# Optimization experiments

Hardware: AMD Instinct MI355X
Metric: run time of the kernel (lower is better)

The kernel has to match this reference:

```python
import jax, jax.numpy as jnp
import numpy as np

S, B, F, D, DF, NH, FH = 1152, 2, 128, 1024, 2048, 8, 4
SEP = 1024
EPS = 1e-5

def ln(x, g, b):
    m = x.mean(-1, keepdims=True)
    v = ((x - m) ** 2).mean(-1, keepdims=True)
    return (x - m) * jax.lax.rsqrt(v + EPS) * g + b

def mha(q, k, v, wi, bi, wo, bo, nh):
    # torch MultiheadAttention, batch_first=False: inputs (L, N, E)
    E = q.shape[-1]
    hd = E // nh
    qh = (q @ wi[:E].T + bi[:E]).reshape(q.shape[0], -1, nh, hd)
    kh = (k @ wi[E:2 * E].T + bi[E:2 * E]).reshape(k.shape[0], -1, nh, hd)
    vh = (v @ wi[2 * E:].T + bi[2 * E:]).reshape(k.shape[0], -1, nh, hd)
    s = jnp.einsum('qnhd,knhd->nhqk', qh, kh) / jnp.sqrt(jnp.float32(hd))
    a = jax.nn.softmax(s, axis=-1)
    o = jnp.einsum('nhqk,knhd->qnhd', a, vh).reshape(q.shape[0], -1, E)
    return o @ wo.T + bo

def setup_inputs() -> dict:
    key = jax.random.key(0)
    it = iter(jax.random.split(key, 40))
    def p(shape, s=0.02):
        return jax.random.normal(next(it), shape, jnp.float32) * s
    z = lambda *sh: jnp.zeros(sh, jnp.float32)
    o = lambda *sh: jnp.ones(sh, jnp.float32)
    return dict(
        src=jax.random.normal(next(it), (S, B, F), jnp.float32),
        sep=SEP,
        sa_wi=p((3 * D, D)), sa_bi=z(3 * D), sa_wo=p((D, D)), sa_bo=z(D),
        fa_wi=p((3 * F, F)), fa_bi=z(3 * F), fa_wo=p((F, F)), fa_bo=z(F),
        pl1_w=p((F, 1)), pl1_b=z(F),
        pl2_w=p((DF, F)), pl2_b=z(DF),
        pl3_w=p((1, DF)), pl3_b=z(1),
        pl4_w=p((DF, F)), pl4_b=z(DF),
        pl5_w=p((D, DF)), pl5_b=z(D),
        pl6_w=p((DF, D)), pl6_b=z(DF),
        pl7_w=p((D, DF)), pl7_b=z(D),
        l1_w=p((DF, D)), l1_b=z(DF),
        l2_w=p((F, DF)), l2_b=z(F),
        pn1_g=o(F), pn1_b=z(F),
        pn2_g=o(D), pn2_b=z(D),
        n1_g=o(D), n1_b=z(D),
        n2_g=o(F), n2_b=z(F),
    )

def _forward(src, sa_wi, sa_bi, sa_wo, sa_bo, fa_wi, fa_bi, fa_wo, fa_bo,
             pl1_w, pl1_b, pl2_w, pl2_b, pl3_w, pl3_b, pl4_w, pl4_b,
             pl5_w, pl5_b, pl6_w, pl6_b, pl7_w, pl7_b, l1_w, l1_b, l2_w, l2_b,
             pn1_g, pn1_b, pn2_g, pn2_b, n1_g, n1_b, n2_g, n2_b, sep):
    Sn, Bn, Fn = src.shape
    relu = jax.nn.relu
    # feature-wise attention: 'b h w -> w (b h) 1'
    x = jnp.transpose(src, (2, 0, 1)).reshape(Fn, Sn * Bn, 1)
    x = x @ pl1_w.T + pl1_b                       # (F, S*B, emsize_f)
    x = mha(x, x, x, fa_wi, fa_bi, fa_wo, fa_bo, FH)
    x = relu(x @ pl2_w.T + pl2_b) @ pl3_w.T + pl3_b  # (F, S*B, 1)
    x = jnp.transpose(x.reshape(Fn, Sn, Bn), (1, 2, 0))  # 'w (b h) 1 -> b h w'
    src1 = ln(x + src, pn1_g, pn1_b)              # (S, B, F)
    src1_ = relu(src1 @ pl4_w.T + pl4_b) @ pl5_w.T + pl5_b  # (S, B, D)
    li = src1_[:sep]
    sl = mha(li, li, li, sa_wi, sa_bi, sa_wo, sa_bo, NH)
    sl = ln(sl + li, pn2_g, pn2_b)
    sl_ = relu(sl @ pl6_w.T + pl6_b) @ pl7_w.T + pl7_b
    sl_ = ln(sl_, pn2_g, pn2_b) + sl
    sr = mha(src1_[sep:], sl_, sl_, sa_wi, sa_bi, sa_wo, sa_bo, NH)
    src2 = jnp.concatenate([sl, sr], axis=0)      # (S, B, D)
    so = ln(src2 + src1_, n1_g, n1_b)
    ff = relu(so @ l1_w.T + l1_b) @ l2_w.T + l2_b  # (S, B, F)
    return ln(src1 + ff, n2_g, n2_b)

def reference(src, sa_wi, sa_bi, sa_wo, sa_bo, fa_wi, fa_bi, fa_wo, fa_bo,
              pl1_w, pl1_b, pl2_w, pl2_b, pl3_w, pl3_b, pl4_w, pl4_b,
              pl5_w, pl5_b, pl6_w, pl6_b, pl7_w, pl7_b, l1_w, l1_b, l2_w, l2_b,
              pn1_g, pn1_b, pn2_g, pn2_b, n1_g, n1_b, n2_g, n2_b, sep):
    return _forward(src, sa_wi, sa_bi, sa_wo, sa_bo, fa_wi, fa_bi, fa_wo, fa_bo,
                    pl1_w, pl1_b, pl2_w, pl2_b, pl3_w, pl3_b, pl4_w, pl4_b,
                    pl5_w, pl5_b, pl6_w, pl6_b, pl7_w, pl7_b, l1_w, l1_b,
                    l2_w, l2_b, pn1_g, pn1_b, pn2_g, pn2_b, n1_g, n1_b,
                    n2_g, n2_b, sep)
```

## Files before the change

### kernel.cpp

```cpp
#include <hip/hip_runtime.h>

using s16x8 = __attribute__((ext_vector_type(8))) short;
using f32x4 = __attribute__((ext_vector_type(4))) float;
typedef unsigned short ushort_t;

__device__ __forceinline__ unsigned short f2bf(float f) {
    union { float f; unsigned u; } v; v.f = f;
    unsigned u = v.u + 0x7FFFu + ((v.u >> 16) & 1u);
    return (unsigned short)(u >> 16);
}
__device__ __forceinline__ float bf2f(unsigned short h) {
    union { unsigned u; float f; } v; v.u = ((unsigned)h) << 16;
    return v.f;
}

__device__ __forceinline__ float block_reduce(float v, int op, float* lds) {
    const int lane = threadIdx.x & 63;
    const int w    = threadIdx.x >> 6;
    const int nw   = blockDim.x >> 6;
#pragma unroll
    for (int off = 32; off > 0; off >>= 1) {
        float o = __shfl_down(v, off, 64);
        v = op ? fmaxf(v, o) : (v + o);
    }
    __syncthreads();
    if (lane == 0) lds[w] = v;
    __syncthreads();
    float r = lds[0];
    for (int i = 1; i < nw; i++) r = op ? fmaxf(r, lds[i]) : (r + lds[i]);
    return r;
}

__device__ __forceinline__ void load_lds16(const void* g, void* l) {
    __builtin_amdgcn_global_load_lds(
        (const __attribute__((address_space(1))) unsigned int*)g,
        (__attribute__((address_space(3))) unsigned int*)l, 16, 0, 0);
}

struct CvtArgs { const float* src[8]; ushort_t* dst[8]; int end[8]; };

__global__ __launch_bounds__(256)
void cvt_all(CvtArgs a)
{
    int i = blockIdx.x * 256 + threadIdx.x;
    int j = 0;
    while (j < 8 && i >= a.end[j]) j++;
    if (j >= 8) return;
    int li = i - (j ? a.end[j - 1] : 0);
    float4 v = *(const float4*)&a.src[j][(size_t)li * 4];
    ushort_t u[4] = { f2bf(v.x), f2bf(v.y), f2bf(v.z), f2bf(v.w) };
    *(uint2*)&a.dst[j][(size_t)li * 4] = *(uint2*)u;
}

template<bool RELU, bool SPLITK>
__global__ __launch_bounds__(256, 2)
void gemm_bf16(const ushort_t* __restrict__ A, const ushort_t* __restrict__ B,
               const float* __restrict__ bias, ushort_t* __restrict__ C,
               float* __restrict__ Cp, long pstride, int ksplen, int zmod,
               int M, int N, int K, int lda, int ldb, int ldc,
               long sAz, long sBz, long sCz, long sA2, long sB2, long sC2,
               int zshift, float alpha)
{
    __shared__ ushort_t As[128 * 32];
    __shared__ ushort_t Bs[128 * 32];

    const int tid = threadIdx.x;
    int zz = blockIdx.z;
    int ks = 0, z = zz;
    if (SPLITK) { ks = zz / zmod; z = zz - ks * zmod; }
    const int z1  = z & ((1 << zshift) - 1);
    const int z2  = z >> zshift;
    const int m0  = blockIdx.x * 128;
    const int n0  = blockIdx.y * 128;

    const ushort_t* Ab = A + (size_t)z1 * sAz + (size_t)z2 * sA2 + (size_t)m0 * lda;
    const ushort_t* Bb = B + (size_t)z1 * sBz + (size_t)z2 * sB2 + (size_t)n0 * ldb;

    const int wave = tid >> 6, lane = tid & 63;
    const int wm = (wave & 1) * 64, wn = (wave >> 1) * 64;
    const int mi = lane & 15, quad = lane >> 4;

    f32x4 acc[4][4];
#pragma unroll
    for (int i = 0; i < 4; i++)
#pragma unroll
        for (int j = 0; j < 4; j++) acc[i][j] = (f32x4)0.f;

    const int r_0 = tid >> 2,           g_0 = (tid & 3) ^ ((r_0 >> 1) & 3);
    const int r_1 = (tid + 256) >> 2,   g_1 = (tid & 3) ^ ((r_1 >> 1) & 3);

    const int kbeg = SPLITK ? ks * ksplen : 0;
    const int kend = SPLITK ? kbeg + ksplen : K;

    for (int k0 = kbeg; k0 < kend; k0 += 32) {
        load_lds16(Ab + (size_t)r_0 * lda + k0 + g_0 * 8, &As[tid * 8]);
        load_lds16(Ab + (size_t)r_1 * lda + k0 + g_1 * 8, &As[(tid + 256) * 8]);
        load_lds16(Bb + (size_t)r_0 * ldb + k0 + g_0 * 8, &Bs[tid * 8]);
        load_lds16(Bb + (size_t)r_1 * ldb + k0 + g_1 * 8, &Bs[(tid + 256) * 8]);
        __syncthreads();

        s16x8 af[4], bfr[4];
#pragma unroll
        for (int t = 0; t < 4; t++) {
            int r = wm + t * 16 + mi;
            af[t] = *(const s16x8*)&As[r * 32 + ((quad ^ ((r >> 1) & 3)) * 8)];
        }
#pragma unroll
        for (int t = 0; t < 4; t++) {
            int r = wn + t * 16 + mi;
            bfr[t] = *(const s16x8*)&Bs[r * 32 + ((quad ^ ((r >> 1) & 3)) * 8)];
        }
#pragma unroll
        for (int tm = 0; tm < 4; tm++)
#pragma unroll
            for (int tn = 0; tn < 4; tn++)
                acc[tm][tn] = __builtin_amdgcn_mfma_f32_16x16x32_bf16(af[tm], bfr[tn], acc[tm][tn], 0, 0, 0);
        __syncthreads();
    }

    if (SPLITK) {
        float* Cf = Cp + (size_t)ks * pstride + (size_t)z1 * sCz + (size_t)z2 * sC2;
#pragma unroll
        for (int tn = 0; tn < 4; tn++) {
            int col = n0 + wn + tn * 16 + mi;
#pragma unroll
            for (int tm = 0; tm < 4; tm++)
#pragma unroll
                for (int r = 0; r < 4; r++) {
                    int row = m0 + wm + tm * 16 + quad * 4 + r;
                    Cf[(size_t)row * ldc + col] = acc[tm][tn][r] * alpha;
                }
        }
    } else {
#pragma unroll
        for (int tn = 0; tn < 4; tn++) {
            int col = n0 + wn + tn * 16 + mi;
            float bv = bias ? bias[col] : 0.f;
#pragma unroll
            for (int tm = 0; tm < 4; tm++) {
#pragma unroll
                for (int r = 0; r < 4; r++) {
                    int row = m0 + wm + tm * 16 + quad * 4 + r;
                    float v = acc[tm][tn][r] * alpha + bv;
                    if (RELU) v = fmaxf(v, 0.f);
                    C[(size_t)z1 * sCz + (size_t)z2 * sC2 + (size_t)row * ldc + col] = f2bf(v);
                }
            }
        }
    }
}

__global__ __launch_bounds__(256)
void sum_cvt(const float* __restrict__ parts, long pstride, int P,
             const float* __restrict__ bias, int ldc,
             ushort_t* __restrict__ out, int total4)
{
    int i = blockIdx.x * 256 + threadIdx.x;
    if (i >= total4) return;
    size_t idx = (size_t)i * 4;
    float4 s = *(const float4*)&parts[idx];
    for (int p = 1; p < P; p++) {
        float4 v = *(const float4*)&parts[(size_t)p * pstride + idx];
        s.x += v.x; s.y += v.y; s.z += v.z; s.w += v.w;
    }
    if (bias) {
        int col = (int)(idx % (size_t)ldc);
        s.x += bias[col]; s.y += bias[col + 1]; s.z += bias[col + 2]; s.w += bias[col + 3];
    }
    ushort_t u[4] = { f2bf(s.x), f2bf(s.y), f2bf(s.z), f2bf(s.w) };
    *(uint2*)&out[idx] = *(uint2*)u;
}

__global__ __launch_bounds__(128)
void ln_part(const float* __restrict__ parts, long pstride, int P,
             const float* __restrict__ bias, const ushort_t* __restrict__ resid,
             const float* __restrict__ g, const float* __restrict__ beta,
             float* __restrict__ out)
{
    __shared__ float red[4];
    const int r = blockIdx.x, c = threadIdx.x;
    float x = bias[c] + bf2f(resid[r * 128 + c]);
    for (int p = 0; p < P; p++) x += parts[(size_t)p * pstride + (size_t)r * 128 + c];
    float s  = block_reduce(x, 0, red);
    float ss = block_reduce(x * x, 0, red);
    float mean = s * (1.f / 128.f);
    float var  = ss * (1.f / 128.f) - mean * mean;
    float inv  = rsqrtf(var + 1e-5f);
    out[(size_t)r * 128 + c] = (x - mean) * inv * g[c] + beta[c];
}

__global__ __launch_bounds__(256)
void transp128(const ushort_t* __restrict__ in, ushort_t* __restrict__ out,
               int ldin, long inz1, long inz2, long outz)
{
    __shared__ ushort_t T[64][136];
    const int z = blockIdx.z, z1 = z & 7, z2 = z >> 3;
    const int n0 = blockIdx.x * 64;
    const ushort_t* ip = in + (size_t)z1 * inz1 + (size_t)z2 * inz2;
    const int rr = threadIdx.x >> 2, cg = (threadIdx.x & 3) * 32;
#pragma unroll
    for (int c = 0; c < 4; c++) {
        s16x8 v = *(const s16x8*)(ip + (size_t)(n0 + rr) * ldin + cg + c * 8);
        *(s16x8*)&T[rr][cg + c * 8] = v;
    }
    __syncthreads();
    const int d = threadIdx.x >> 1, j0 = (threadIdx.x & 1) * 32;
    ushort_t* op = out + (size_t)z * outz + (size_t)d * 1024 + n0 + j0;
#pragma unroll
    for (int c = 0; c < 4; c++) {
        s16x8 v;
#pragma unroll
        for (int j = 0; j < 8; j++) v[j] = (short)T[j0 + c * 8 + j][d];
        *(s16x8*)(op + c * 8) = v;
    }
}

__global__ void precomp1(const float* __restrict__ fa_wi, const float* __restrict__ fa_bi,
                         const float* __restrict__ pl1_w, const float* __restrict__ pl1_b,
                         float* __restrict__ consts)
{
    int j = threadIdx.x;
    if (j < 384) {
        float u = 0.f, v = 0.f;
        for (int k = 0; k < 128; k++) {
            float w = fa_wi[j * 128 + k];
            u = fmaf(w, pl1_w[k], u);
            v = fmaf(w, pl1_b[k], v);
        }
        consts[j]       = u;
        consts[512 + j] = v + fa_bi[j];
    }
}

__global__ void precomp2(const float* __restrict__ fa_wo, const float* __restrict__ fa_bo,
                         float* __restrict__ consts)
{
    int tid = threadIdx.x;
    const float* u = consts;
    const float* v = consts + 512;
    if (tid < 16) {
        int h = tid >> 2, w = tid & 3;
        const float* ql = (w < 2) ? u : v;
        const float* kr = ((w & 1) == 0) ? u : v;
        float acc = 0.f;
        for (int d = 0; d < 32; d++) acc += ql[h * 32 + d] * kr[128 + h * 32 + d];
        consts[1024 + tid] = acc * 0.17677669529663687f;
    }
#pragma unroll
    for (int h = 0; h < 4; h++) {
        float acc = 0.f;
        for (int d = 0; d < 32; d++)
            acc = fmaf(fa_wo[tid * 128 + h * 32 + d], u[256 + h * 32 + d], acc);
        consts[1088 + h * 128 + tid] = acc;
    }
    float c0 = fa_bo[tid];
    for (int idx = 0; idx < 128; idx++)
        c0 = fmaf(fa_wo[tid * 128 + idx], v[256 + idx], c0);
    consts[1600 + tid] = c0;
}

__global__ void precomp3(const float* __restrict__ pl2_w, const float* __restrict__ pl2_b,
                         const float* __restrict__ consts, ushort_t* __restrict__ Gb)
{
    int m = blockIdx.x * 256 + threadIdx.x;
    const float* wv = consts + 1088;
    const float* c0 = consts + 1600;
    float a0 = 0.f, ah[4] = {0.f, 0.f, 0.f, 0.f};
    for (int j = 0; j < 128; j++) {
        float w = pl2_w[m * 128 + j];
        ah[0] = fmaf(w, wv[0 * 128 + j], ah[0]);
        ah[1] = fmaf(w, wv[1 * 128 + j], ah[1]);
        ah[2] = fmaf(w, wv[2 * 128 + j], ah[2]);
        ah[3] = fmaf(w, wv[3 * 128 + j], ah[3]);
        a0    = fmaf(w, c0[j], a0);
    }
    ushort_t row[8];
#pragma unroll
    for (int h = 0; h < 4; h++) row[h] = f2bf(ah[h]);
    row[4] = f2bf(a0 + pl2_b[m]);
    row[5] = row[6] = row[7] = 0;
    *(uint4*)&Gb[m * 8] = *(uint4*)row;
}

__global__ __launch_bounds__(512, 4)
void feat_mlp_ln(const float* __restrict__ src, const float* __restrict__ consts,
                 const ushort_t* __restrict__ Gb, const float* __restrict__ pl3_w,
                 const float* __restrict__ pl3_b, const float* __restrict__ pn1_g,
                 const float* __restrict__ pn1_b, ushort_t* __restrict__ src1)
{
    __shared__ ushort_t Gs[2048 * 8];
    __shared__ ushort_t Ts[128 * 8];
    __shared__ float    sv[128];
    __shared__ float    ypart[4][128];
    __shared__ float    red[8];

    const int n   = blockIdx.x;
    const int tid = threadIdx.x;
    const int f   = tid & 127;
    const int h   = tid >> 7;
    const bool act = (tid < 128);

#pragma unroll
    for (int p = 0; p < 4; p++) {
        int ci = tid + p * 512;
        load_lds16(Gb + (size_t)ci * 8, &Gs[ci * 8]);
    }
    if (act) sv[f] = src[n * 128 + f];
    __syncthreads();

    const float si = sv[f];
    float S1 = block_reduce(act ? si : 0.f, 0, red);
    float S2 = block_reduce(act ? si * si : 0.f, 0, red);
    float S3 = block_reduce(act ? si * si * si : 0.f, 0, red);
    float S4 = block_reduce(act ? si * si * si * si : 0.f, 0, red);
    float amax = block_reduce(act ? fabsf(si) : 0.f, 1, red);

    const float p_ = consts[1024 + h * 4 + 0] * si + consts[1024 + h * 4 + 2];
    float pmax = block_reduce(fabsf(p_), 1, red);

    float tt;
    if (pmax * amax < 0.25f) {
        float num = fmaf(p_, fmaf(p_, fmaf(p_, S4 * (1.f / 6.f), 0.5f * S3), S2), S1);
        float den = fmaf(p_, fmaf(p_, fmaf(p_, S3 * (1.f / 6.f), 0.5f * S2), S1), 128.f);
        tt = num / den;
    } else {
        float smax = block_reduce(act ? si : -3.4e38f, 1, red);
        float smin = -block_reduce(act ? -si : -3.4e38f, 1, red);
        float m = fmaxf(p_ * smax, p_ * smin);
        float l = 0.f, t = 0.f;
        for (int j = 0; j < 128; j++) {
            float e = __expf(fmaf(p_, sv[j], -m));
            l += e; t = fmaf(e, sv[j], t);
        }
        tt = t / l;
    }

    Ts[f * 8 + h] = f2bf(tt);
    if (act) {
        Ts[f * 8 + 4] = 0x3F80;
        Ts[f * 8 + 5] = 0; Ts[f * 8 + 6] = 0; Ts[f * 8 + 7] = 0;
    }
    __syncthreads();

    const int wave = tid >> 6, lane = tid & 63;
    const int wm = (wave & 1) * 64;
    const int mq = wave >> 1;
    const int mi = lane & 15, quad = lane >> 4;

    s16x8 af[4];
#pragma unroll
    for (int t = 0; t < 4; t++) {
        s16x8 v = *(const s16x8*)&Ts[(wm + t * 16 + mi) * 8];
        af[t] = (quad == 0) ? v : (s16x8)0;
    }

    float partial[4][4];
#pragma unroll
    for (int i = 0; i < 4; i++)
#pragma unroll
        for (int j = 0; j < 4; j++) partial[i][j] = 0.f;

#pragma unroll 4
    for (int mt = 0; mt < 32; mt++) {
        const int m0 = mq * 512 + mt * 16;
        s16x8 bfr = *(const s16x8*)&Gs[(m0 + mi) * 8];
        float w = pl3_w[m0 + mi];
        f32x4 acc[4];
#pragma unroll
        for (int tm = 0; tm < 4; tm++)
            acc[tm] = __builtin_amdgcn_mfma_f32_16x16x32_bf16(af[tm], bfr, (f32x4)0.f, 0, 0, 0);
#pragma unroll
        for (int tm = 0; tm < 4; tm++)
#pragma unroll
            for (int r = 0; r < 4; r++)
                partial[tm][r] = fmaf(fmaxf(acc[tm][r], 0.f), w, partial[tm][r]);
    }

#pragma unroll
    for (int tm = 0; tm < 4; tm++)
#pragma unroll
        for (int r = 0; r < 4; r++) {
            float v = partial[tm][r];
            v += __shfl_xor(v, 8);
            v += __shfl_xor(v, 4);
            v += __shfl_xor(v, 2);
            v += __shfl_xor(v, 1);
            if (mi == 0) ypart[mq][wm + tm * 16 + quad * 4 + r] = v;
        }
    __syncthreads();

    float yv = 0.f;
    if (act)
        yv = ypart[0][f] + ypart[1][f] + ypart[2][f] + ypart[3][f] + pl3_b[0] + sv[f];
    float s  = block_reduce(yv, 0, red);
    float ss = block_reduce(yv * yv, 0, red);
    float mean = s * (1.f / 128.f);
    float var  = ss * (1.f / 128.f) - mean * mean;
    float inv  = rsqrtf(var + 1e-5f);
    if (act)
        src1[n * 128 + f] = f2bf((yv - mean) * inv * pn1_g[f] + pn1_b[f]);
}

template<bool OUTF32>
__global__ void ln_bf16(const ushort_t* __restrict__ a, const ushort_t* __restrict__ b,
                        const ushort_t* __restrict__ post, const float* __restrict__ g,
                        const float* __restrict__ beta, void* __restrict__ out, int D)
{
    __shared__ float red[4];
    const size_t row = blockIdx.x;
    const int tid = threadIdx.x;
    const int nit = D / blockDim.x;
    const ushort_t* ap = a + row * D;
    const ushort_t* bp = b ? b + row * D : nullptr;
    float xr[4];
    float s = 0.f, ss = 0.f;
    for (int i = 0; i < nit; i++) {
        int idx = i * blockDim.x + tid;
        float x = bf2f(ap[idx]) + (bp ? bf2f(bp[idx]) : 0.f);
        xr[i] = x; s += x; ss = fmaf(x, x, ss);
    }
    s  = block_reduce(s, 0, red);
    ss = block_reduce(ss, 0, red);
    float mean = s / D, var = ss / D - mean * mean;
    float inv = rsqrtf(var + 1e-5f);
    const ushort_t* pp = post ? post + row * D : nullptr;
    for (int i = 0; i < nit; i++) {
        int idx = i * blockDim.x + tid;
        float v = (xr[i] - mean) * inv * g[idx] + beta[idx];
        if (pp) v += bf2f(pp[idx]);
        if (OUTF32) ((float*)out)[row * D + idx] = v;
        else        ((ushort_t*)out)[row * D + idx] = f2bf(v);
    }
}

__global__ void ln_cat(const ushort_t* __restrict__ a1, const ushort_t* __restrict__ a2,
                       int split, const ushort_t* __restrict__ b,
                       const float* __restrict__ g, const float* __restrict__ beta,
                       ushort_t* __restrict__ out, int D)
{
    __shared__ float red[4];
    const int row = blockIdx.x;
    const int tid = threadIdx.x;
    const int nit = D / blockDim.x;
    const ushort_t* ap = (row < split) ? a1 + (size_t)row * D : a2 + (size_t)(row - split) * D;
    const ushort_t* bp = b + (size_t)row * D;
    float xr[4];
    float s = 0.f, ss = 0.f;
    for (int i = 0; i < nit; i++) {
        int idx = i * blockDim.x + tid;
        float x = bf2f(ap[idx]) + bf2f(bp[idx]);
        xr[i] = x; s += x; ss = fmaf(x, x, ss);
    }
    s  = block_reduce(s, 0, red);
    ss = block_reduce(ss, 0, red);
    float mean = s / D, var = ss / D - mean * mean;
    float inv = rsqrtf(var + 1e-5f);
    for (int i = 0; i < nit; i++) {
        int idx = i * blockDim.x + tid;
        out[(size_t)row * D + idx] = f2bf((xr[i] - mean) * inv * g[idx] + beta[idx]);
    }
}

__global__ __launch_bounds__(256)
void softmax_bf16(ushort_t* __restrict__ S)
{
    __shared__ float red[4];
    const size_t row = blockIdx.x;
    ushort_t* p = S + row * 1024;
    const int tid = threadIdx.x;
    uint2 u = *(const uint2*)&p[tid * 4];
    ushort_t* us = (ushort_t*)&u;
    float xr[4];
    float mx = -3.4e38f;
#pragma unroll
    for (int i = 0; i < 4; i++) { xr[i] = bf2f(us[i]); mx = fmaxf(mx, xr[i]); }
    mx = block_reduce(mx, 1, red);
    float sum = 0.f;
#pragma unroll
    for (int i = 0; i < 4; i++) { xr[i] = __expf(xr[i] - mx); sum += xr[i]; }
    sum = block_reduce(sum, 0, red);
    float inv = 1.f / sum;
#pragma unroll
    for (int i = 0; i < 4; i++) us[i] = f2bf(xr[i] * inv);
    *(uint2*)&p[tid * 4] = u;
}

static inline void gemm_go(hipStream_t s, const ushort_t* A, const ushort_t* B,
                           const float* bias, ushort_t* C,
                           int M, int N, int K, int lda, int ldb, int ldc,
                           long sAz, long sBz, long sCz, int Z, float alpha,
                           bool relu,
                           long sA2 = 0, long sB2 = 0, long sC2 = 0, int zshift = 0,
                           int ksplit = 1, float* Cp = nullptr, long pstride = 0)
{
    dim3 g(M / 128, N / 128, Z * ksplit), b(256);
    int ksplen = K / ksplit;
    if (ksplit > 1)
        gemm_bf16<false, true ><<<g, b, 0, s>>>(A, B, nullptr, nullptr, Cp, pstride, ksplen, Z,
            M, N, K, lda, ldb, ldc, sAz, sBz, sCz, sA2, sB2, sC2, zshift, alpha);
    else if (relu)
        gemm_bf16<true,  false><<<g, b, 0, s>>>(A, B, bias, C, nullptr, 0, 0, Z,
            M, N, K, lda, ldb, ldc, sAz, sBz, sCz, sA2, sB2, sC2, zshift, alpha);
    else
        gemm_bf16<false, false><<<g, b, 0, s>>>(A, B, bias, C, nullptr, 0, 0, Z,
            M, N, K, lda, ldb, ldc, sAz, sBz, sCz, sA2, sB2, sC2, zshift, alpha);
}

extern "C" void kernel_launch(void* const* d_in, const int* in_sizes, int n_in,
                              void* d_out, int out_size, void* d_ws, size_t ws_size,
                              hipStream_t stream)
{
    const float* src   = (const float*)d_in[0];
    const float* sa_wi = (const float*)d_in[2];
    const float* sa_bi = (const float*)d_in[3];
    const float* sa_wo = (const float*)d_in[4];
    const float* sa_bo = (const float*)d_in[5];
    const float* fa_wi = (const float*)d_in[6];
    const float* fa_bi = (const float*)d_in[7];
    const float* fa_wo = (const float*)d_in[8];
    const float* fa_bo = (const float*)d_in[9];
    const float* pl1_w = (const float*)d_in[10];
    const float* pl1_b = (const float*)d_in[11];
    const float* pl2_w = (const float*)d_in[12];
    const float* pl2_b = (const float*)d_in[13];
    const float* pl3_w = (const float*)d_in[14];
    const float* pl3_b = (const float*)d_in[15];
    const float* pl4_w = (const float*)d_in[16];
    const float* pl4_b = (const float*)d_in[17];
    const float* pl5_w = (const float*)d_in[18];
    const float* pl5_b = (const float*)d_in[19];
    const float* pl6_w = (const float*)d_in[20];
    const float* pl6_b = (const float*)d_in[21];
    const float* pl7_w = (const float*)d_in[22];
    const float* pl7_b = (const float*)d_in[23];
    const float* l1_w  = (const float*)d_in[24];
    const float* l1_b  = (const float*)d_in[25];
    const float* l2_w  = (const float*)d_in[26];
    const float* l2_b  = (const float*)d_in[27];
    const float* pn1_g = (const float*)d_in[28];
    const float* pn1_b = (const float*)d_in[29];
    const float* pn2_g = (const float*)d_in[30];
    const float* pn2_b = (const float*)d_in[31];
    const float* n1_g  = (const float*)d_in[32];
    const float* n1_b  = (const float*)d_in[33];
    const float* n2_g  = (const float*)d_in[34];
    const float* n2_b  = (const float*)d_in[35];

    float* ws  = (float*)d_ws;
    float* out = (float*)d_out;

    float* CONSTS = ws;
    ushort_t* wsb = (ushort_t*)(ws + 16384);
    ushort_t* SAWIb  = wsb + 0;
    ushort_t* SAWOb  = wsb + 3145728;
    ushort_t* PL4b   = wsb + 4194304;
    ushort_t* PL5b   = wsb + 4456448;
    ushort_t* PL6b   = wsb + 6553600;
    ushort_t* PL7b   = wsb + 8650752;
    ushort_t* L1b    = wsb + 10747904;
    ushort_t* L2b    = wsb + 12845056;
    ushort_t* Gbb    = wsb + 13107200;
    ushort_t* SRC1b  = wsb + 13172736;
    ushort_t* HBIGb  = wsb + 13467648;
    ushort_t* SRC1_b = wsb + 18186240;
    ushort_t* QKVb   = wsb + 20545536;
    ushort_t* SBUFb  = wsb + 27623424;
    ushort_t* OBUFb  = wsb + 44400640;
    ushort_t* SLb    = wsb + 46497792;
    ushort_t* SLPb   = wsb + 48594944;
    ushort_t* SOb    = wsb + 50692096;
    float* PARTS = (float*)SBUFb;

    {
        CvtArgs a;
        const float* srcs[8] = { sa_wi, sa_wo, pl4_w, pl5_w, pl6_w, pl7_w, l1_w, l2_w };
        ushort_t*    dsts[8] = { SAWIb, SAWOb, PL4b, PL5b, PL6b, PL7b, L1b, L2b };
        int          ns[8]   = { 3145728, 1048576, 262144, 2097152, 2097152, 2097152, 2097152, 262144 };
        int cum = 0;
        for (int i = 0; i < 8; i++) { a.src[i] = srcs[i]; a.dst[i] = dsts[i]; cum += ns[i] / 4; a.end[i] = cum; }
        cvt_all<<<(cum + 255) / 256, 256, 0, stream>>>(a);
    }

    precomp1<<<1, 384, 0, stream>>>(fa_wi, fa_bi, pl1_w, pl1_b, CONSTS);
    precomp2<<<1, 128, 0, stream>>>(fa_wo, fa_bo, CONSTS);
    precomp3<<<8, 256, 0, stream>>>(pl2_w, pl2_b, CONSTS, Gbb);
    feat_mlp_ln<<<2304, 512, 0, stream>>>(src, CONSTS, Gbb, pl3_w, pl3_b, pn1_g, pn1_b, SRC1b);

    gemm_go(stream, SRC1b, PL4b, pl4_b, HBIGb, 2304, 2048, 128, 128, 128, 2048, 0, 0, 0, 1, 1.f, true);
    gemm_go(stream, HBIGb, PL5b, nullptr, nullptr, 2304, 1024, 2048, 2048, 2048, 1024, 0, 0, 0, 1, 1.f, false,
            0, 0, 0, 0, 2, PARTS, 2359296);
    sum_cvt<<<2304, 256, 0, stream>>>(PARTS, 2359296, 2, pl5_b, 1024, SRC1_b, 589824);

    gemm_go(stream, SRC1_b, SAWIb, sa_bi, QKVb, 2304, 3072, 1024, 1024, 1024, 3072, 0, 0, 0, 1, 1.f, false);
    const float iscale = 0.08838834764831845f;
    ushort_t* VT1 = HBIGb;
    transp128<<<dim3(16, 1, 16), 256, 0, stream>>>(QKVb + 2048, VT1, 6144, 128, 3072, 131072);
    gemm_go(stream, QKVb, QKVb + 1024, nullptr, SBUFb,
            1024, 1024, 128, 6144, 6144, 1024, 128, 128, 1048576, 16, iscale, false,
            3072, 3072, 8388608, 3);
    softmax_bf16<<<16384, 256, 0, stream>>>(SBUFb);
    gemm_go(stream, SBUFb, VT1, nullptr, OBUFb,
            1024, 128, 1024, 1024, 1024, 2048, 1048576, 131072, 128, 16, 1.f, false,
            8388608, 1048576, 1024, 3);
    gemm_go(stream, OBUFb, SAWOb, sa_bo, HBIGb, 2048, 1024, 1024, 1024, 1024, 1024, 0, 0, 0, 1, 1.f, false);
    ln_bf16<false><<<2048, 256, 0, stream>>>(HBIGb, SRC1_b, nullptr, pn2_g, pn2_b, SLb, 1024);

    gemm_go(stream, SLb, PL6b, pl6_b, HBIGb, 2048, 2048, 1024, 1024, 1024, 2048, 0, 0, 0, 1, 1.f, true);
    gemm_go(stream, HBIGb, PL7b, pl7_b, OBUFb, 2048, 1024, 2048, 2048, 2048, 1024, 0, 0, 0, 1, 1.f, false);
    ln_bf16<false><<<2048, 256, 0, stream>>>(OBUFb, nullptr, SLb, pn2_g, pn2_b, SLPb, 1024);

    ushort_t* KV2 = SBUFb;
    ushort_t* S2  = SBUFb + 4456448;
    ushort_t* SR  = SBUFb + 6553600;
    gemm_go(stream, SLPb, SAWIb + 1024 * 1024, sa_bi + 1024, KV2, 2048, 2048, 1024, 1024, 1024, 2048, 0, 0, 0, 1, 1.f, false);
    ushort_t* VT2 = HBIGb;
    transp128<<<dim3(16, 1, 16), 256, 0, stream>>>(KV2 + 1024, VT2, 4096, 128, 2048, 131072);
    gemm_go(stream, QKVb + 2048 * 3072, KV2, nullptr, S2,
            128, 1024, 128, 6144, 4096, 1024, 128, 128, 131072, 16, iscale, false,
            3072, 2048, 1048576, 3);
    softmax_bf16<<<2048, 256, 0, stream>>>(S2);
    gemm_go(stream, S2, VT2, nullptr, nullptr,
            128, 128, 1024, 1024, 1024, 2048, 131072, 131072, 128, 16, 1.f, false,
            1048576, 1048576, 1024, 3, 8, PARTS, 262144);
    sum_cvt<<<256, 256, 0, stream>>>(PARTS, 262144, 8, nullptr, 2048, OBUFb, 65536);
    gemm_go(stream, OBUFb, SAWOb, nullptr, nullptr, 256, 1024, 1024, 1024, 1024, 1024, 0, 0, 0, 1, 1.f, false,
            0, 0, 0, 0, 8, PARTS, 262144);
    sum_cvt<<<256, 256, 0, stream>>>(PARTS, 262144, 8, sa_bo, 1024, SR, 65536);

    ln_cat<<<2304, 256, 0, stream>>>(SLb, SR, 2048, SRC1_b, n1_g, n1_b, SOb, 1024);

    gemm_go(stream, SOb, L1b, l1_b, HBIGb, 2304, 2048, 1024, 1024, 1024, 2048, 0, 0, 0, 1, 1.f, true);
    gemm_go(stream, HBIGb, L2b, nullptr, nullptr, 2304, 128, 2048, 2048, 2048, 128, 0, 0, 0, 1, 1.f, false,
            0, 0, 0, 0, 8, PARTS, 294912);
    ln_part<<<2304, 128, 0, stream>>>(PARTS, 294912, 8, l2_b, SRC1b, n2_g, n2_b, out);
}
```

Baseline: 591.0 us.

## Split-K the mid-size GEMMs and fuse bias/ReLU into partial-sum reduction

Four more large GEMMs (attention out-projection, pl6, pl7, l1) now use split-K=2, writing fp32 partials that a templated sum_cvt kernel reduces while adding bias and an optional ReLU before converting to bf16. The aim is more workgroups per GEMM to fill the GPU. In feat_mlp_ln, pl3_w is staged into LDS, the ReLU-weighted accumulation uses packed 2-wide float ops, and the occupancy hint is raised from 4 to 6. In exchange, the split-K path adds fp32 partial writes and reads plus an extra kernel launch per GEMM, which may cost more than the added parallelism gains for GEMMs that already have many tiles.

```diff
diff --git a/kernel.cpp b/kernel.cpp
--- a/kernel.cpp
+++ b/kernel.cpp
@@ -2,6 +2,7 @@
 
 using s16x8 = __attribute__((ext_vector_type(8))) short;
 using f32x4 = __attribute__((ext_vector_type(4))) float;
+using f32x2 = __attribute__((ext_vector_type(2))) float;
 typedef unsigned short ushort_t;
 
 __device__ __forceinline__ unsigned short f2bf(float f) {
@@ -150,6 +151,7 @@
     }
 }
 
+template<bool RELU>
 __global__ __launch_bounds__(256)
 void sum_cvt(const float* __restrict__ parts, long pstride, int P,
              const float* __restrict__ bias, int ldc,
@@ -166,6 +168,10 @@
     if (bias) {
         int col = (int)(idx % (size_t)ldc);
         s.x += bias[col]; s.y += bias[col + 1]; s.z += bias[col + 2]; s.w += bias[col + 3];
+    }
+    if (RELU) {
+        s.x = fmaxf(s.x, 0.f); s.y = fmaxf(s.y, 0.f);
+        s.z = fmaxf(s.z, 0.f); s.w = fmaxf(s.w, 0.f);
     }
     ushort_t u[4] = { f2bf(s.x), f2bf(s.y), f2bf(s.z), f2bf(s.w) };
     *(uint2*)&out[idx] = *(uint2*)u;
@@ -282,13 +288,14 @@
     *(uint4*)&Gb[m * 8] = *(uint4*)row;
 }
 
-__global__ __launch_bounds__(512, 4)
+__global__ __launch_bounds__(512, 6)
 void feat_mlp_ln(const float* __restrict__ src, const float* __restrict__ consts,
                  const ushort_t* __restrict__ Gb, const float* __restrict__ pl3_w,
                  const float* __restrict__ pl3_b, const float* __restrict__ pn1_g,
                  const float* __restrict__ pn1_b, ushort_t* __restrict__ src1)
 {
     __shared__ ushort_t Gs[2048 * 8];
+    __shared__ float    wlds[2048];
     __shared__ ushort_t Ts[128 * 8];
     __shared__ float    sv[128];
     __shared__ float    ypart[4][128];
@@ -305,6 +312,7 @@
         int ci = tid + p * 512;
         load_lds16(Gb + (size_t)ci * 8, &Gs[ci * 8]);
     }
+    load_lds16(pl3_w + tid * 4, &wlds[tid * 4]);
     if (act) sv[f] = src[n * 128 + f];
     __syncthreads();
 
@@ -354,33 +362,37 @@
         af[t] = (quad == 0) ? v : (s16x8)0;
     }
 
-    float partial[4][4];
-#pragma unroll
-    for (int i = 0; i < 4; i++)
-#pragma unroll
-        for (int j = 0; j < 4; j++) partial[i][j] = 0.f;
+    f32x2 partial2[4][2];
+#pragma unroll
+    for (int i = 0; i < 4; i++) { partial2[i][0] = (f32x2)0.f; partial2[i][1] = (f32x2)0.f; }
+    const f32x2 zero2 = (f32x2)0.f;
 
 #pragma unroll 4
     for (int mt = 0; mt < 32; mt++) {
         const int m0 = mq * 512 + mt * 16;
         s16x8 bfr = *(const s16x8*)&Gs[(m0 + mi) * 8];
-        float w = pl3_w[m0 + mi];
+        float w = wlds[m0 + mi];
+        f32x2 w2 = { w, w };
         f32x4 acc[4];
 #pragma unroll
         for (int tm = 0; tm < 4; tm++)
             acc[tm] = __builtin_amdgcn_mfma_f32_16x16x32_bf16(af[tm], bfr, (f32x4)0.f, 0, 0, 0);
 #pragma unroll
-        for (int tm = 0; tm < 4; tm++)
-#pragma unroll
-            for (int r = 0; r < 4; r++)
-                partial[tm][r] = fmaf(fmaxf(acc[tm][r], 0.f), w, partial[tm][r]);
+        for (int tm = 0; tm < 4; tm++) {
+            f32x2* pa = (f32x2*)&acc[tm];
+#pragma unroll
+            for (int i = 0; i < 2; i++) {
+                f32x2 r = __builtin_elementwise_max(pa[i], zero2);
+                partial2[tm][i] = r * w2 + partial2[tm][i];
+            }
+        }
     }
 
 #pragma unroll
     for (int tm = 0; tm < 4; tm++)
 #pragma unroll
         for (int r = 0; r < 4; r++) {
-            float v = partial[tm][r];
+            float v = partial2[tm][r >> 1][r & 1];
             v += __shfl_xor(v, 8);
             v += __shfl_xor(v, 4);
             v += __shfl_xor(v, 2);
@@ -589,7 +601,7 @@
     gemm_go(stream, SRC1b, PL4b, pl4_b, HBIGb, 2304, 2048, 128, 128, 128, 2048, 0, 0, 0, 1, 1.f, true);
     gemm_go(stream, HBIGb, PL5b, nullptr, nullptr, 2304, 1024, 2048, 2048, 2048, 1024, 0, 0, 0, 1, 1.f, false,
             0, 0, 0, 0, 2, PARTS, 2359296);
-    sum_cvt<<<2304, 256, 0, stream>>>(PARTS, 2359296, 2, pl5_b, 1024, SRC1_b, 589824);
+    sum_cvt<false><<<2304, 256, 0, stream>>>(PARTS, 2359296, 2, pl5_b, 1024, SRC1_b, 589824);
 
     gemm_go(stream, SRC1_b, SAWIb, sa_bi, QKVb, 2304, 3072, 1024, 1024, 1024, 3072, 0, 0, 0, 1, 1.f, false);
     const float iscale = 0.08838834764831845f;
@@ -602,11 +614,17 @@
     gemm_go(stream, SBUFb, VT1, nullptr, OBUFb,
             1024, 128, 1024, 1024, 1024, 2048, 1048576, 131072, 128, 16, 1.f, false,
             8388608, 1048576, 1024, 3);
-    gemm_go(stream, OBUFb, SAWOb, sa_bo, HBIGb, 2048, 1024, 1024, 1024, 1024, 1024, 0, 0, 0, 1, 1.f, false);
+    gemm_go(stream, OBUFb, SAWOb, nullptr, nullptr, 2048, 1024, 1024, 1024, 1024, 1024, 0, 0, 0, 1, 1.f, false,
+            0, 0, 0, 0, 2, PARTS, 2097152);
+    sum_cvt<false><<<2048, 256, 0, stream>>>(PARTS, 2097152, 2, sa_bo, 1024, HBIGb, 524288);
     ln_bf16<false><<<2048, 256, 0, stream>>>(HBIGb, SRC1_b, nullptr, pn2_g, pn2_b, SLb, 1024);
 
-    gemm_go(stream, SLb, PL6b, pl6_b, HBIGb, 2048, 2048, 1024, 1024, 1024, 2048, 0, 0, 0, 1, 1.f, true);
-    gemm_go(stream, HBIGb, PL7b, pl7_b, OBUFb, 2048, 1024, 2048, 2048, 2048, 1024, 0, 0, 0, 1, 1.f, false);
+    gemm_go(stream, SLb, PL6b, nullptr, nullptr, 2048, 2048, 1024, 1024, 1024, 2048, 0, 0, 0, 1, 1.f, false,
+            0, 0, 0, 0, 2, PARTS, 4194304);
+    sum_cvt<true><<<4096, 256, 0, stream>>>(PARTS, 4194304, 2, pl6_b, 2048, HBIGb, 1048576);
+    gemm_go(stream, HBIGb, PL7b, nullptr, nullptr, 2048, 1024, 2048, 2048, 2048, 1024, 0, 0, 0, 1, 1.f, false,
+            0, 0, 0, 0, 2, PARTS, 2097152);
+    sum_cvt<false><<<2048, 256, 0, stream>>>(PARTS, 2097152, 2, pl7_b, 1024, OBUFb, 524288);
     ln_bf16<false><<<2048, 256, 0, stream>>>(OBUFb, nullptr, SLb, pn2_g, pn2_b, SLPb, 1024);
 
     ushort_t* KV2 = SBUFb;
@@ -622,14 +640,16 @@
     gemm_go(stream, S2, VT2, nullptr, nullptr,
             128, 128, 1024, 1024, 1024, 2048, 131072, 131072, 128, 16, 1.f, false,
             1048576, 1048576, 1024, 3, 8, PARTS, 262144);
-    sum_cvt<<<256, 256, 0, stream>>>(PARTS, 262144, 8, nullptr, 2048, OBUFb, 65536);
+    sum_cvt<false><<<256, 256, 0, stream>>>(PARTS, 262144, 8, nullptr, 2048, OBUFb, 65536);
     gemm_go(stream, OBUFb, SAWOb, nullptr, nullptr, 256, 1024, 1024, 1024, 1024, 1024, 0, 0, 0, 1, 1.f, false,
             0, 0, 0, 0, 8, PARTS, 262144);
-    sum_cvt<<<256, 256, 0, stream>>>(PARTS, 262144, 8, sa_bo, 1024, SR, 65536);
+    sum_cvt<false><<<256, 256, 0, stream>>>(PARTS, 262144, 8, sa_bo, 1024, SR, 65536);
 
     ln_cat<<<2304, 256, 0, stream>>>(SLb, SR, 2048, SRC1_b, n1_g, n1_b, SOb, 1024);
 
-    gemm_go(stream, SOb, L1b, l1_b, HBIGb, 2304, 2048, 1024, 1024, 1024, 2048, 0, 0, 0, 1, 1.f, true);
+    gemm_go(stream, SOb, L1b, nullptr, nullptr, 2304, 2048, 1024, 1024, 1024, 2048, 0, 0, 0, 1, 1.f, false,
+            0, 0, 0, 0, 2, PARTS, 4718592);
+    sum_cvt<true><<<4608, 256, 0, stream>>>(PARTS, 4718592, 2, l1_b, 2048, HBIGb, 1179648);
     gemm_go(stream, HBIGb, L2b, nullptr, nullptr, 2304, 128, 2048, 2048, 2048, 128, 0, 0, 0, 1, 1.f, false,
             0, 0, 0, 0, 8, PARTS, 294912);
     ln_part<<<2304, 128, 0, stream>>>(PARTS, 294912, 8, l2_b, SRC1b, n2_g, n2_b, out);
```

Result: no change. 589.0 us (-0.3%).
